# Kernel optimization log

Measured on AMD Instinct MI355X. Metric: run time of the kernel, lower is better.

Reference implementation:

```python
import jax, jax.numpy as jnp
import numpy as np
from jax import lax

N, CIN, H, W = 32, 128, 64, 64
COUT, KH, KW = 256, 3, 3
STRIDE = (1, 1)
PADDING = ((1, 1), (1, 1))


def setup_inputs() -> dict:
    key = jax.random.key(0)
    k1, k2, k3, k4 = jax.random.split(key, 4)
    # binary input in {0,1}
    x = jax.random.randint(k1, (N, CIN, H, W), 0, 2).astype(jnp.float32)
    # ternary weight in {-1,0,1}
    weight = (jax.random.randint(k2, (COUT, CIN, KH, KW), 0, 3) - 1).astype(jnp.float32)
    # integer bias (folded from BN, floored to int per get_sign_bias_from_bn)
    bias = jax.random.randint(k3, (COUT,), -200, 200).astype(jnp.float32)
    # sign in {-1,+1}, broadcast shape (1, COUT, 1, 1)
    sign = jnp.where(jax.random.bernoulli(k4, 0.5, (1, COUT, 1, 1)), 1.0, -1.0).astype(jnp.float32)
    return {"x": x, "weight": weight, "bias": bias, "sign": sign}


def reference(x, weight, bias, sign):
    # y = conv2d(x, W) + bias  (stride 1, pad 1, NCHW)
    y = lax.conv_general_dilated(
        x, weight,
        window_strides=STRIDE,
        padding=PADDING,
        dimension_numbers=("NCHW", "OIHW", "NCHW"),
    ) + bias[None, :, None, None]
    # rounding=True -> torch.round_(y)
    y = jnp.round(y)
    # output = 1 iff sign * y >= 0, cast back to input dtype
    return jnp.where(y * sign >= 0, jnp.float32(1), jnp.float32(0)).astype(x.dtype)
```

## Files before the change

### kernel.cpp

```cpp
#include <hip/hip_runtime.h>
#include <cstdint>


#define NIMG 32
#define CIN  128
#define HH   64
#define WW   64
#define COUT 256
#define PH   66
#define XT_ROWSTRIDE (PH * CIN)
#define XT_NSTRIDE   (PH * PH * CIN)
#define XT_BYTES     ((size_t)NIMG * XT_NSTRIDE)
#define WP_TAPSTRIDE (COUT * CIN)
#define WP_BYTES     ((size_t)9 * WP_TAPSTRIDE)

typedef int v4i __attribute__((ext_vector_type(4)));

__global__ __launch_bounds__(256) void xt_prepass(const float* __restrict__ x,
                                                  int8_t* __restrict__ xt) {
    const int py = blockIdx.x;
    const int n  = blockIdx.y;
    const int t  = threadIdx.x;
    int8_t* rowbase = xt + (size_t)(n * PH + py) * XT_ROWSTRIDE;

    if (py == 0 || py == PH - 1) {
        int4 z = {0, 0, 0, 0};
        for (int j = t; j < XT_ROWSTRIDE / 16; j += 256)
            ((int4*)rowbase)[j] = z;
        return;
    }

    __shared__ __align__(16) int8_t Ls[64 * 144];
    const int y  = py - 1;
    const int xq = t & 15;
    const float4* xf = (const float4*)x;
#pragma unroll
    for (int j = 0; j < 8; ++j) {
        const int ci = (t >> 4) + j * 16;
        float4 v = xf[((size_t)(n * CIN + ci) * HH + y) * 16 + xq];
        const int xv = xq * 4;
        Ls[(xv + 0) * 144 + ci] = (int8_t)v.x;
        Ls[(xv + 1) * 144 + ci] = (int8_t)v.y;
        Ls[(xv + 2) * 144 + ci] = (int8_t)v.z;
        Ls[(xv + 3) * 144 + ci] = (int8_t)v.w;
    }
    __syncthreads();
    const int4 z = {0, 0, 0, 0};
    for (int j = t; j < XT_ROWSTRIDE / 16; j += 256) {
        const int px  = j >> 3;
        const int col = (j & 7) * 16;
        int4 val;
        if (px == 0 || px == PH - 1) val = z;
        else                         val = *(const int4*)&Ls[(px - 1) * 144 + col];
        *(int4*)(rowbase + (size_t)j * 16) = val;
    }
}

__global__ __launch_bounds__(256) void w_prepack(const float* __restrict__ w,
                                                 int8_t* __restrict__ wp) {
    const int idx = blockIdx.x * 256 + threadIdx.x;
    if (idx >= (int)WP_BYTES) return;
    const int tap = idx >> 15;
    const int rem = idx & 32767;
    const int co  = rem >> 7;
    const int ci  = rem & 127;
    wp[idx] = (int8_t)w[(size_t)(co * CIN + ci) * 9 + tap];
}

__device__ __forceinline__ void glds16(const void* g, uint32_t lds_off) {
    asm volatile("s_mov_b32 m0, %0\n"
                 "global_load_lds_dwordx4 %1, off"
                 :: "s"(lds_off), "v"(g) : "memory");
}

__global__ __launch_bounds__(256) void binconv_gemm(
    const int8_t* __restrict__ xt, const int8_t* __restrict__ wp,
    const float* __restrict__ bias, const float* __restrict__ sign,
    float* __restrict__ out) {

    __shared__ __align__(16) int8_t smem[2 * 128 * 64];
    int8_t* Ws = smem;
    int8_t* Xs = smem + 8192;

    const int t    = threadIdx.x;
    const int wid  = t >> 6;
    const int lane = t & 63;
    const int bx   = blockIdx.x;
    const int co0  = blockIdx.y * 128;
    const int n    = bx >> 5;
    const int y0   = (bx & 31) << 1;

    const int8_t* xg = xt + (size_t)n * XT_NSTRIDE + (size_t)y0 * XT_ROWSTRIDE
                     + (size_t)(t >> 2) * CIN + (t & 3) * 16;
    const int8_t* wg = wp + (size_t)(co0 + (t >> 2)) * CIN + (t & 3) * 16;

    const uint32_t ldsW0 = __builtin_amdgcn_readfirstlane(
        (uint32_t)(uintptr_t)Ws + (uint32_t)(wid * 1024));
    const uint32_t ldsX0 = __builtin_amdgcn_readfirstlane(
        (uint32_t)(uintptr_t)Xs + (uint32_t)(wid * 1024));

    v4i acc[4][4] = {};

    const int row    = lane & 15;
    const int quad   = lane >> 4;
    const int co_off = (wid >> 1) * 64;
    const int m_off  = (wid & 1) * 64;

#pragma unroll
    for (int tap = 0; tap < 9; ++tap) {
        const int ky = tap / 3, kx = tap % 3;
        const int8_t* xgt = xg + (ky * PH + kx) * CIN;
        const int8_t* wgt = wg + tap * WP_TAPSTRIDE;
#pragma unroll
        for (int half = 0; half < 2; ++half) {
            __syncthreads();
            glds16(xgt + half * 64,                ldsX0);
            glds16(xgt + half * 64 + XT_ROWSTRIDE, ldsX0 + 4096);
            glds16(wgt + half * 64,                ldsW0);
            glds16(wgt + half * 64 + 64 * CIN,     ldsW0 + 4096);
            asm volatile("s_waitcnt vmcnt(0)" ::: "memory");
            __syncthreads();

            v4i af[4], bf[4];
#pragma unroll
            for (int c = 0; c < 4; ++c)
                af[c] = *(const v4i*)&Ws[(co_off + c * 16 + row) * 64 + quad * 16];
#pragma unroll
            for (int m = 0; m < 4; ++m)
                bf[m] = *(const v4i*)&Xs[(m_off + m * 16 + row) * 64 + quad * 16];
#pragma unroll
            for (int c = 0; c < 4; ++c)
#pragma unroll
                for (int m = 0; m < 4; ++m)
                    acc[c][m] = __builtin_amdgcn_mfma_i32_16x16x64_i8(
                        af[c], bf[m], acc[c][m], 0, 0, 0);
        }
    }

    const float* bco = bias + co0 + co_off;
    const float* sco = sign + co0 + co_off;
    float* outb = out + ((size_t)n * COUT + co0 + co_off) * (HH * WW)
                + y0 * WW + m_off;
#pragma unroll
    for (int c = 0; c < 4; ++c) {
#pragma unroll
        for (int r = 0; r < 4; ++r) {
            const int col_co = c * 16 + quad * 4 + r;
            const float bv = bco[col_co];
            const float sv = sco[col_co];
            float* orow = outb + (size_t)col_co * (HH * WW);
#pragma unroll
            for (int m = 0; m < 4; ++m) {
                const float yv = (float)acc[c][m][r] + bv;
                const bool on = (sv > 0.0f) ? (yv >= 0.0f) : (yv <= 0.0f);
                orow[m * 16 + row] = on ? 1.0f : 0.0f;
            }
        }
    }
}

__global__ __launch_bounds__(256) void naive_conv(
    const float* __restrict__ x, const float* __restrict__ w,
    const float* __restrict__ bias, const float* __restrict__ sign,
    float* __restrict__ out) {
    const int idx = blockIdx.x * 256 + threadIdx.x;
    const int xc = idx & 63, y = (idx >> 6) & 63, co = (idx >> 12) & 255,
              n = idx >> 20;
    float s = 0.f;
    for (int ci = 0; ci < CIN; ++ci)
        for (int ky = 0; ky < 3; ++ky) {
            const int iy = y + ky - 1;
            if (iy < 0 || iy >= HH) continue;
            for (int kx = 0; kx < 3; ++kx) {
                const int ix = xc + kx - 1;
                if (ix < 0 || ix >= WW) continue;
                s += x[((size_t)(n * CIN + ci) * HH + iy) * WW + ix] *
                     w[((size_t)(co * CIN + ci) * 3 + ky) * 3 + kx];
            }
        }
    const float yv = s + bias[co];
    out[idx] = ((sign[co] > 0.f) ? (yv >= 0.f) : (yv <= 0.f)) ? 1.0f : 0.0f;
}

extern "C" void kernel_launch(void* const* d_in, const int* in_sizes, int n_in,
                              void* d_out, int out_size, void* d_ws, size_t ws_size,
                              hipStream_t stream) {
    const float* x    = (const float*)d_in[0];
    const float* w    = (const float*)d_in[1];
    const float* bias = (const float*)d_in[2];
    const float* sign = (const float*)d_in[3];
    float* out = (float*)d_out;

    const size_t need = XT_BYTES + WP_BYTES;
    if (ws_size < need) {
        naive_conv<<<dim3((NIMG * COUT * HH * WW) / 256), 256, 0, stream>>>(
            x, w, bias, sign, out);
        return;
    }
    int8_t* xt = (int8_t*)d_ws;
    int8_t* wp = (int8_t*)d_ws + XT_BYTES;

    xt_prepass<<<dim3(PH, NIMG), 256, 0, stream>>>(x, xt);
    w_prepack<<<dim3((int)(WP_BYTES + 255) / 256), 256, 0, stream>>>(w, wp);
    binconv_gemm<<<dim3(NIMG * (HH / 2), COUT / 128), 256, 0, stream>>>(
        xt, wp, bias, sign, out);
}
```

Before: 234.6 us.

## Stage four padded input rows in LDS once and read weights directly from global

```diff
diff --git a/kernel.cpp b/kernel.cpp
--- a/kernel.cpp
+++ b/kernel.cpp
@@ -78,9 +78,7 @@
     const float* __restrict__ bias, const float* __restrict__ sign,
     float* __restrict__ out) {
 
-    __shared__ __align__(16) int8_t smem[2 * 128 * 64];
-    int8_t* Ws = smem;
-    int8_t* Xs = smem + 8192;
+    __shared__ __align__(16) int8_t Xraw[4 * XT_ROWSTRIDE];
 
     const int t    = threadIdx.x;
     const int wid  = t >> 6;
@@ -90,44 +88,41 @@
     const int n    = bx >> 5;
     const int y0   = (bx & 31) << 1;
 
-    const int8_t* xg = xt + (size_t)n * XT_NSTRIDE + (size_t)y0 * XT_ROWSTRIDE
-                     + (size_t)(t >> 2) * CIN + (t & 3) * 16;
-    const int8_t* wg = wp + (size_t)(co0 + (t >> 2)) * CIN + (t & 3) * 16;
-
-    const uint32_t ldsW0 = __builtin_amdgcn_readfirstlane(
-        (uint32_t)(uintptr_t)Ws + (uint32_t)(wid * 1024));
-    const uint32_t ldsX0 = __builtin_amdgcn_readfirstlane(
-        (uint32_t)(uintptr_t)Xs + (uint32_t)(wid * 1024));
-
-    v4i acc[4][4] = {};
+    const int8_t* xbase = xt + (size_t)n * XT_NSTRIDE + (size_t)y0 * XT_ROWSTRIDE;
+    {
+        const int8_t* gsrc = xbase + lane * 16;
+        const uint32_t lds0 = (uint32_t)(uintptr_t)Xraw;
+        for (int j = wid; j < 33; j += 4)
+            glds16(gsrc + j * 1024,
+                   __builtin_amdgcn_readfirstlane(lds0 + j * 1024));
+        asm volatile("s_waitcnt vmcnt(0)" ::: "memory");
+        __syncthreads();
+    }
 
     const int row    = lane & 15;
     const int quad   = lane >> 4;
     const int co_off = (wid >> 1) * 64;
     const int m_off  = (wid & 1) * 64;
 
+    const int8_t* wbase = wp + (size_t)(co0 + co_off + row) * CIN + quad * 16;
+    const int8_t* xlbase = Xraw + (wid & 1) * XT_ROWSTRIDE + row * CIN + quad * 16;
+
+    v4i acc[4][4] = {};
+
 #pragma unroll
     for (int tap = 0; tap < 9; ++tap) {
         const int ky = tap / 3, kx = tap % 3;
-        const int8_t* xgt = xg + (ky * PH + kx) * CIN;
-        const int8_t* wgt = wg + tap * WP_TAPSTRIDE;
+        const int8_t* wt = wbase + tap * WP_TAPSTRIDE;
+        const int8_t* xl = xlbase + ky * XT_ROWSTRIDE + kx * CIN;
 #pragma unroll
         for (int half = 0; half < 2; ++half) {
-            __syncthreads();
-            glds16(xgt + half * 64,                ldsX0);
-            glds16(xgt + half * 64 + XT_ROWSTRIDE, ldsX0 + 4096);
-            glds16(wgt + half * 64,                ldsW0);
-            glds16(wgt + half * 64 + 64 * CIN,     ldsW0 + 4096);
-            asm volatile("s_waitcnt vmcnt(0)" ::: "memory");
-            __syncthreads();
-
             v4i af[4], bf[4];
 #pragma unroll
             for (int c = 0; c < 4; ++c)
-                af[c] = *(const v4i*)&Ws[(co_off + c * 16 + row) * 64 + quad * 16];
+                af[c] = *(const v4i*)(wt + half * 64 + c * 16 * CIN);
 #pragma unroll
             for (int m = 0; m < 4; ++m)
-                bf[m] = *(const v4i*)&Xs[(m_off + m * 16 + row) * 64 + quad * 16];
+                bf[m] = *(const v4i*)(xl + half * 64 + m * 16 * CIN);
 #pragma unroll
             for (int c = 0; c < 4; ++c)
 #pragma unroll
```

Result: slower. 267.3 us (+13.9%).
